# Kernel tuning notes

Hardware: AMD Instinct MI355X
Metric: run time of the kernel (lower is better)

Reference implementation:

```python
import jax, jax.numpy as jnp
import numpy as np

N_NODES = 50000
IN_CH = 512
OUT_CH = 128
N_EDGES = 1_600_000


def setup_inputs() -> dict:
    key = jax.random.key(0)
    k1, k2, k3, k4 = jax.random.split(key, 4)
    x = jax.random.normal(k1, (N_NODES, IN_CH), dtype=jnp.float32)
    edge_index = jax.random.randint(k2, (2, N_EDGES), 0, N_NODES, dtype=jnp.int64)
    # GCNConv params (weight [in, out], bias [out]); decoder Linear(out, in, bias=False) -> weight [in, out] used as z @ W_dec
    W_enc = jax.random.normal(k3, (IN_CH, OUT_CH), dtype=jnp.float32) * 0.05
    b_enc = jnp.zeros((OUT_CH,), dtype=jnp.float32)
    W_dec = jax.random.normal(k4, (OUT_CH, IN_CH), dtype=jnp.float32) * 0.05
    return {"x": x, "edge_index": edge_index, "W_enc": W_enc, "b_enc": b_enc, "W_dec": W_dec}


def reference(x, edge_index, W_enc, b_enc, W_dec):
    N = x.shape[0]
    # --- GCNConv: add self-loops, symmetric normalization, gather-scale-scatter ---
    loops = jnp.arange(N, dtype=edge_index.dtype)
    src = jnp.concatenate([edge_index[0], loops])  # message sources
    dst = jnp.concatenate([edge_index[1], loops])  # aggregation targets
    deg = jax.ops.segment_sum(jnp.ones_like(dst, dtype=x.dtype), dst, num_segments=N)
    deg_inv_sqrt = jnp.where(deg > 0, jax.lax.rsqrt(jnp.maximum(deg, 1.0)), 0.0)
    norm = deg_inv_sqrt[src] * deg_inv_sqrt[dst]  # [E+N]
    xw = x @ W_enc                                 # [N, OUT]
    msg = xw[src] * norm[:, None]                  # gather + scale
    z = jax.ops.segment_sum(msg, dst, num_segments=N) + b_enc  # scatter-add
    # --- decode head: relu -> linear (no bias) -> softmax over features ---
    z = jax.nn.relu(z)
    logits = z @ W_dec                             # [N, IN]
    return jax.nn.softmax(logits, axis=1)
```

## Files before the change

kernel.cpp:

```cpp
#include <hip/hip_runtime.h>
#include <stdint.h>

#define NN   50000
#define INC  512
#define OUTC 128
#define NB   782
#define CAP  4096
#define NWG  256

typedef unsigned int  uint;
typedef unsigned short u16;
typedef short bf16x8 __attribute__((ext_vector_type(8)));
typedef float f32x4  __attribute__((ext_vector_type(4)));
typedef u16   u16x8  __attribute__((ext_vector_type(8)));
typedef u16   u16x4  __attribute__((ext_vector_type(4)));

__device__ __forceinline__ u16 f2bf(float f) {
  uint u = __float_as_uint(f);
  u += 0x7fffu + ((u >> 16) & 1u);
  return (u16)(u >> 16);
}
__device__ __forceinline__ float bflo(uint v) { return __uint_as_float(v << 16); }
__device__ __forceinline__ float bfhi(uint v) { return __uint_as_float(v & 0xffff0000u); }

__device__ __forceinline__ void gl_lds16(const void* g, void* l) {
  __builtin_amdgcn_global_load_lds(
      (const __attribute__((address_space(1))) uint*)g,
      (__attribute__((address_space(3))) uint*)l, 16, 0, 0);
}

__global__ __launch_bounds__(256) void k_scatter_pairs(const int* __restrict__ src,
                                                       const int* __restrict__ dst, int E,
                                                       uint* __restrict__ bucket_cursor,
                                                       uint* __restrict__ pairs) {
  __shared__ uint hist[NB];
  __shared__ uint base[NB];
  __shared__ uint cur[NB];
  const int t = threadIdx.x;
  const int chunk = (E + NWG - 1) / NWG;
  const int e0 = blockIdx.x * chunk;
  const int e1 = min(e0 + chunk, E);

  for (int i = t; i < NB; i += 256) hist[i] = 0;
  __syncthreads();
  for (int e = e0 + t; e < e1; e += 256) {
    int b = dst[e] >> 6;
    atomicAdd(&hist[b], 1u);
  }
  __syncthreads();
  for (int i = t; i < NB; i += 256) {
    uint c = hist[i];
    base[i] = c ? atomicAdd(&bucket_cursor[i * 16], c) : 0u;
    cur[i] = 0;
  }
  __syncthreads();
  for (int e = e0 + t; e < e1; e += 256) {
    int d = dst[e];
    int b = d >> 6;
    uint r = atomicAdd(&cur[b], 1u);
    uint off = base[b] + r;
    if (off < CAP) pairs[(size_t)b * CAP + off] = (uint)src[e] | ((uint)(d & 63) << 16);
  }
}

__global__ __launch_bounds__(256) void k_sort(const uint* __restrict__ bucket_cursor,
                                              const uint* __restrict__ pairs,
                                              uint* __restrict__ csr,
                                              uint* __restrict__ rs_packed,
                                              float* __restrict__ dis) {
  __shared__ uint plist[CAP];
  __shared__ uint slist[CAP];
  __shared__ uint cnt[64], pfx[64], cur[64];
  const int b = blockIdx.x, t = threadIdx.x;
  uint n_e = bucket_cursor[b * 16]; if (n_e > CAP) n_e = CAP;

  if (t < 64) cnt[t] = 0;
  __syncthreads();
  for (uint e = t; e < n_e; e += 256) {
    uint v = pairs[(size_t)b * CAP + e];
    plist[e] = v;
    atomicAdd(&cnt[(v >> 16) & 63u], 1u);
  }
  __syncthreads();
  if (t == 0) {
    uint run = 0;
    for (int i = 0; i < 64; ++i) { pfx[i] = run; run += cnt[i]; }
  }
  __syncthreads();
  if (t < 64) {
    cur[t] = pfx[t];
    int n = b * 64 + t;
    if (n < NN) {
      rs_packed[n] = pfx[t] | (cnt[t] << 16);
      dis[n] = rsqrtf((float)cnt[t] + 1.0f);
    }
  }
  __syncthreads();
  for (uint e = t; e < n_e; e += 256) {
    uint v = plist[e];
    uint pos = atomicAdd(&cur[(v >> 16) & 63u], 1u);
    slist[pos] = v & 0xffffu;
  }
  __syncthreads();
  for (uint e = t; e < n_e; e += 256) csr[(size_t)b * CAP + e] = slist[e];
}

__global__ __launch_bounds__(256) void k_prep(const float* __restrict__ We,
                                              const float* __restrict__ Wd,
                                              uint8_t* __restrict__ oE,
                                              uint8_t* __restrict__ oD) {
  __shared__ float t[4096];
  const int tid = threadIdx.x;
  if (blockIdx.x < 16) {
    const int k0 = blockIdx.x * 32;
#pragma unroll
    for (int r = 0; r < 16; ++r) {
      int e = r * 256 + tid;
      int kk = e >> 7, n = e & 127;
      t[kk * 128 + n] = We[(size_t)(k0 + kk) * 128 + n];
    }
    __syncthreads();
#pragma unroll
    for (int it = 0; it < 2; ++it) {
      int item = it * 256 + tid;
      int n = item & 127, kc = item >> 7;
      int kg = k0 + kc * 8;
      int q = kg >> 7, kin = kg & 127;
      u16x8 p;
#pragma unroll
      for (int j = 0; j < 8; ++j) p[j] = f2bf(t[(kc * 8 + j) * 128 + n]);
      *(u16x8*)(oE + q * 32768 + ((((uint)n * 256) + (uint)kin * 2) ^ (uint)((n & 7) << 4))) = p;
    }
  } else {
    const int n0 = (blockIdx.x - 16) * 32;
#pragma unroll
    for (int r = 0; r < 16; ++r) {
      int e = r * 256 + tid;
      int k = e >> 5, nl = e & 31;
      t[k * 32 + nl] = Wd[(size_t)k * 512 + n0 + nl];
    }
    __syncthreads();
#pragma unroll
    for (int it = 0; it < 2; ++it) {
      int item = it * 256 + tid;
      int nl = item & 31, kc = item >> 5;
      int n = n0 + nl;
      int c = n >> 7, nin = n & 127;
      u16x8 p;
#pragma unroll
      for (int j = 0; j < 8; ++j) p[j] = f2bf(t[(kc * 8 + j) * 32 + nl]);
      *(u16x8*)(oD + c * 32768 + ((((uint)nin * 256) + (uint)kc * 16) ^ (uint)((nin & 7) << 4))) = p;
    }
  }
}

__global__ __launch_bounds__(256, 2) void k_gemm1(const float* __restrict__ x,
                                                  const uint8_t* __restrict__ WtE,
                                                  const float* __restrict__ dis,
                                                  u16* __restrict__ xws) {
  __shared__ __align__(16) uint8_t lds[49152];
  uint8_t* WL = lds;
  uint8_t* XL = lds + 32768;
  const int tid = threadIdx.x, lane = tid & 63, wv = tid >> 6;
  const int lane15 = lane & 15, laneh = lane >> 4;
  const int rb = blockIdx.x * 128;

  f32x4 acc[2][8];
#pragma unroll
  for (int m = 0; m < 2; ++m)
#pragma unroll
    for (int n = 0; n < 8; ++n) acc[m][n] = (f32x4){0.f, 0.f, 0.f, 0.f};

  const int srow = tid >> 1;
  int grow = rb + srow; if (grow >= NN) grow = NN - 1;
  const int khalf = (tid & 1) * 32;
  const uint xb  = (uint)srow * 128 + (uint)khalf * 2;
  const uint xsw = (uint)((srow & 7) << 4);
  const int ar0 = wv * 32 + lane15, ar1 = ar0 + 16;

  for (int q = 0; q < 4; ++q) {
    __syncthreads();
    { const uint8_t* s = WtE + q * 32768;
#pragma unroll
      for (int i = 0; i < 8; ++i)
        gl_lds16(s + tid * 16 + i * 4096, WL + tid * 16 + i * 4096); }
#pragma unroll
    for (int step = 0; step < 2; ++step) {
      if (step) __syncthreads();
      const float4* xs = (const float4*)(x + (size_t)grow * INC + q * 128 + step * 64 + khalf);
      float4 v[8];
#pragma unroll
      for (int j = 0; j < 8; ++j) v[j] = xs[j];
#pragma unroll
      for (int j = 0; j < 8; ++j) {
        u16x4 p; p.x = f2bf(v[j].x); p.y = f2bf(v[j].y); p.z = f2bf(v[j].z); p.w = f2bf(v[j].w);
        *(u16x4*)(XL + ((xb + j * 8) ^ xsw)) = p;
      }
      __syncthreads();
#pragma unroll
      for (int kk = 0; kk < 2; ++kk) {
        bf16x8 a0 = *(const bf16x8*)(XL + (((uint)ar0 * 128 + kk * 64 + laneh * 16) ^ (uint)((ar0 & 7) << 4)));
        bf16x8 a1 = *(const bf16x8*)(XL + (((uint)ar1 * 128 + kk * 64 + laneh * 16) ^ (uint)((ar1 & 7) << 4)));
#pragma unroll
        for (int nf = 0; nf < 8; ++nf) {
          int n = nf * 16 + lane15;
          bf16x8 b = *(const bf16x8*)(WL + (((uint)n * 256 + step * 128 + kk * 64 + laneh * 16) ^ (uint)((n & 7) << 4)));
          acc[0][nf] = __builtin_amdgcn_mfma_f32_16x16x32_bf16(a0, b, acc[0][nf], 0, 0, 0);
          acc[1][nf] = __builtin_amdgcn_mfma_f32_16x16x32_bf16(a1, b, acc[1][nf], 0, 0, 0);
        }
      }
    }
  }
#pragma unroll
  for (int m = 0; m < 2; ++m) {
#pragma unroll
    for (int r = 0; r < 4; ++r) {
      int row = rb + wv * 32 + m * 16 + laneh * 4 + r;
      if (row < NN) {
        float dv = dis[row];
#pragma unroll
        for (int nf = 0; nf < 8; ++nf)
          xws[(size_t)row * 128 + nf * 16 + lane15] = f2bf(acc[m][nf][r] * dv);
      }
    }
  }
}

__global__ __launch_bounds__(128) void k_aggregate(const u16* __restrict__ xws,
                                                   const float* __restrict__ dis,
                                                   const uint* __restrict__ rs_packed,
                                                   const uint* __restrict__ csr,
                                                   const float* __restrict__ bias,
                                                   uint8_t* __restrict__ zsw) {
  const int i = blockIdx.x * 2 + (threadIdx.x >> 6);
  const int lane = threadIdx.x & 63;
  const uint v = rs_packed[i];
  const uint s0 = (uint)(i >> 6) * CAP + (v & 0xffffu);
  const uint s1 = s0 + (v >> 16);

  float a0 = 0.f, a1 = 0.f;
  uint j = s0;
  for (; j + 7 < s1; j += 8) {
    uint idx[8], vv[8];
#pragma unroll
    for (int t = 0; t < 8; ++t) idx[t] = csr[j + t];
#pragma unroll
    for (int t = 0; t < 8; ++t) vv[t] = *(const uint*)(xws + (size_t)idx[t] * 128 + lane * 2);
#pragma unroll
    for (int t = 0; t < 8; ++t) { a0 += bflo(vv[t]); a1 += bfhi(vv[t]); }
  }
  for (; j < s1; ++j) {
    uint vv = *(const uint*)(xws + (size_t)csr[j] * 128 + lane * 2);
    a0 += bflo(vv); a1 += bfhi(vv);
  }
  uint vs = *(const uint*)(xws + (size_t)i * 128 + lane * 2);
  float di = dis[i];
  float2 bb = *(const float2*)(bias + lane * 2);
  float z0 = fmaxf(di * (a0 + bflo(vs)) + bb.x, 0.f);
  float z1 = fmaxf(di * (a1 + bfhi(vs)) + bb.y, 0.f);
  uint pk = (uint)f2bf(z0) | ((uint)f2bf(z1) << 16);
  *(uint*)(zsw + ((((uint)i * 256) + (uint)lane * 4) ^ (uint)((i & 7) << 4))) = pk;
}

__global__ __launch_bounds__(256, 2) void k_decode(const uint8_t* __restrict__ zsw,
                                                   const uint8_t* __restrict__ WtD,
                                                   float* __restrict__ out) {
  __shared__ __align__(16) uint8_t lds[49152];
  uint8_t* ZL = lds;
  uint8_t* WL = lds + 16384;
  const int tid = threadIdx.x, lane = tid & 63, wv = tid >> 6;
  const int lane15 = lane & 15, laneh = lane >> 4;
  const int rb = blockIdx.x * 64;

  { const uint8_t* s = zsw + (size_t)rb * 256;
#pragma unroll
    for (int i = 0; i < 4; ++i)
      gl_lds16(s + tid * 16 + i * 4096, ZL + tid * 16 + i * 4096); }

  f32x4 acc[32];
#pragma unroll
  for (int f = 0; f < 32; ++f) acc[f] = (f32x4){0.f, 0.f, 0.f, 0.f};

  const int zr = wv * 16 + lane15;
  bf16x8 a[4];

#pragma unroll
  for (int c = 0; c < 4; ++c) {
    if (c) __syncthreads();
    { const uint8_t* s = WtD + c * 32768;
#pragma unroll
      for (int i = 0; i < 8; ++i)
        gl_lds16(s + tid * 16 + i * 4096, WL + tid * 16 + i * 4096); }
    __syncthreads();
    if (c == 0) {
#pragma unroll
      for (int s = 0; s < 4; ++s)
        a[s] = *(const bf16x8*)(ZL + (((uint)zr * 256 + s * 64 + laneh * 16) ^ (uint)((zr & 7) << 4)));
    }
#pragma unroll
    for (int nf = 0; nf < 8; ++nf) {
      int n = nf * 16 + lane15;
      uint nb = (uint)n * 256 + laneh * 16, nsw = (uint)((n & 7) << 4);
#pragma unroll
      for (int s = 0; s < 4; ++s) {
        bf16x8 bfr = *(const bf16x8*)(WL + ((nb + s * 64) ^ nsw));
        acc[c * 8 + nf] = __builtin_amdgcn_mfma_f32_16x16x32_bf16(a[s], bfr, acc[c * 8 + nf], 0, 0, 0);
      }
    }
  }

#pragma unroll
  for (int r = 0; r < 4; ++r) {
    float m = acc[0][r];
#pragma unroll
    for (int f = 1; f < 32; ++f) m = fmaxf(m, acc[f][r]);
    m = fmaxf(m, __shfl_xor(m, 1)); m = fmaxf(m, __shfl_xor(m, 2));
    m = fmaxf(m, __shfl_xor(m, 4)); m = fmaxf(m, __shfl_xor(m, 8));
    float sum = 0.f;
#pragma unroll
    for (int f = 0; f < 32; ++f) { acc[f][r] = __expf(acc[f][r] - m); sum += acc[f][r]; }
    sum += __shfl_xor(sum, 1); sum += __shfl_xor(sum, 2);
    sum += __shfl_xor(sum, 4); sum += __shfl_xor(sum, 8);
    float inv = 1.0f / sum;
    int row = rb + wv * 16 + laneh * 4 + r;
    if (row < NN) {
      float* op = out + (size_t)row * INC + lane15;
#pragma unroll
      for (int f = 0; f < 32; ++f)
        op[(f >> 3) * 128 + (f & 7) * 16] = acc[f][r] * inv;
    }
  }
}

extern "C" void kernel_launch(void* const* d_in, const int* in_sizes, int n_in,
                              void* d_out, int out_size, void* d_ws, size_t ws_size,
                              hipStream_t stream) {
  const float* x     = (const float*)d_in[0];
  const int*   ei    = (const int*)d_in[1];
  const float* W_enc = (const float*)d_in[2];
  const float* b_enc = (const float*)d_in[3];
  const float* W_dec = (const float*)d_in[4];
  float* out = (float*)d_out;

  const int E = in_sizes[1] / 2;
  const int* esrc = ei;
  const int* edst = ei + E;

  uint8_t* ws = (uint8_t*)d_ws;
  uint*  bucket_cursor = (uint*)(ws);
  uint*  pairs         = (uint*)(ws + 0x10000);
  uint*  csr           = (uint*)(ws + 0xC80000);
  uint*  rs_packed     = (uint*)(ws + 0x1900000);
  float* dis           = (float*)(ws + 0x1940000);
  uint8_t* WtE         = ws + 0x1980000;
  uint8_t* WtD         = ws + 0x19A0000;
  u16*   xws           = (u16*)(ws + 0x19C0000);
  uint8_t* zsw         = ws + 0x2600000;

  hipMemsetAsync(bucket_cursor, 0, NB * 64, stream);
  k_scatter_pairs<<<NWG, 256, 0, stream>>>(esrc, edst, E, bucket_cursor, pairs);
  k_sort         <<<NB, 256, 0, stream>>>(bucket_cursor, pairs, csr, rs_packed, dis);
  k_prep         <<<32, 256, 0, stream>>>(W_enc, W_dec, WtE, WtD);
  k_gemm1        <<<(NN + 127) / 128, 256, 0, stream>>>(x, WtE, dis, xws);
  k_aggregate    <<<NN / 2, 128, 0, stream>>>(xws, dis, rs_packed, csr, b_enc, zsw);
  k_decode       <<<(NN + 63) / 64, 256, 0, stream>>>(zsw, WtD, out);
}
```

Baseline: 339.7 us.

## Make encoder and decoder GEMMs persistent with whole weight resident in LDS

Both GEMM kernels become persistent: 256 blocks of 512 threads each load the full 128 KB bf16 weight into LDS once. Each wave then walks a contiguous range of 16-row fragments, loading activations straight from global into registers with no LDS staging and no per-K barriers. The encoder also uses the packed v_cvt_pk_bf16_f32 conversion. This removes repeated weight reloads and barrier overhead, at the cost of one block per CU because of the LDS footprint, less latency hiding for the global activation loads, and uncoalesced per-lane row reads of x.

```diff
diff --git a/kernel.cpp b/kernel.cpp
--- a/kernel.cpp
+++ b/kernel.cpp
@@ -7,13 +7,13 @@
 #define NB   782
 #define CAP  4096
 #define NWG  256
+#define NFRAG 3125
 
 typedef unsigned int  uint;
 typedef unsigned short u16;
 typedef short bf16x8 __attribute__((ext_vector_type(8)));
 typedef float f32x4  __attribute__((ext_vector_type(4)));
 typedef u16   u16x8  __attribute__((ext_vector_type(8)));
-typedef u16   u16x4  __attribute__((ext_vector_type(4)));
 
 __device__ __forceinline__ u16 f2bf(float f) {
   uint u = __float_as_uint(f);
@@ -22,6 +22,18 @@
 }
 __device__ __forceinline__ float bflo(uint v) { return __uint_as_float(v << 16); }
 __device__ __forceinline__ float bfhi(uint v) { return __uint_as_float(v & 0xffff0000u); }
+
+__device__ __forceinline__ uint pkbf(float lo, float hi) {
+  uint r;
+  asm("v_cvt_pk_bf16_f32 %0, %1, %2" : "=v"(r) : "v"(lo), "v"(hi));
+  return r;
+}
+__device__ __forceinline__ bf16x8 pack8(float4 a, float4 b) {
+  union { uint u[4]; bf16x8 v; } c;
+  c.u[0] = pkbf(a.x, a.y); c.u[1] = pkbf(a.z, a.w);
+  c.u[2] = pkbf(b.x, b.y); c.u[3] = pkbf(b.z, b.w);
+  return c.v;
+}
 
 __device__ __forceinline__ void gl_lds16(const void* g, void* l) {
   __builtin_amdgcn_global_load_lds(
@@ -154,74 +166,60 @@
   }
 }
 
-__global__ __launch_bounds__(256, 2) void k_gemm1(const float* __restrict__ x,
+__global__ __launch_bounds__(512, 2) void k_gemm1(const float* __restrict__ x,
                                                   const uint8_t* __restrict__ WtE,
                                                   const float* __restrict__ dis,
                                                   u16* __restrict__ xws) {
-  __shared__ __align__(16) uint8_t lds[49152];
-  uint8_t* WL = lds;
-  uint8_t* XL = lds + 32768;
+  __shared__ __align__(16) uint8_t WL[131072];
   const int tid = threadIdx.x, lane = tid & 63, wv = tid >> 6;
   const int lane15 = lane & 15, laneh = lane >> 4;
-  const int rb = blockIdx.x * 128;
-
-  f32x4 acc[2][8];
-#pragma unroll
-  for (int m = 0; m < 2; ++m)
-#pragma unroll
-    for (int n = 0; n < 8; ++n) acc[m][n] = (f32x4){0.f, 0.f, 0.f, 0.f};
-
-  const int srow = tid >> 1;
-  int grow = rb + srow; if (grow >= NN) grow = NN - 1;
-  const int khalf = (tid & 1) * 32;
-  const uint xb  = (uint)srow * 128 + (uint)khalf * 2;
-  const uint xsw = (uint)((srow & 7) << 4);
-  const int ar0 = wv * 32 + lane15, ar1 = ar0 + 16;
-
-  for (int q = 0; q < 4; ++q) {
-    __syncthreads();
-    { const uint8_t* s = WtE + q * 32768;
-#pragma unroll
-      for (int i = 0; i < 8; ++i)
-        gl_lds16(s + tid * 16 + i * 4096, WL + tid * 16 + i * 4096); }
-#pragma unroll
-    for (int step = 0; step < 2; ++step) {
-      if (step) __syncthreads();
-      const float4* xs = (const float4*)(x + (size_t)grow * INC + q * 128 + step * 64 + khalf);
-      float4 v[8];
-#pragma unroll
-      for (int j = 0; j < 8; ++j) v[j] = xs[j];
-#pragma unroll
-      for (int j = 0; j < 8; ++j) {
-        u16x4 p; p.x = f2bf(v[j].x); p.y = f2bf(v[j].y); p.z = f2bf(v[j].z); p.w = f2bf(v[j].w);
-        *(u16x4*)(XL + ((xb + j * 8) ^ xsw)) = p;
+
+#pragma unroll
+  for (int i = 0; i < 16; ++i)
+    gl_lds16(WtE + tid * 16 + i * 8192, WL + tid * 16 + i * 8192);
+  __syncthreads();
+
+  const int s = blockIdx.x * 8 + wv;
+  const int f0 = (s * NFRAG) >> 11, f1 = ((s + 1) * NFRAG) >> 11;
+
+  for (int f = f0; f < f1; ++f) {
+    const float* xr = x + (size_t)(f * 16 + lane15) * INC + laneh * 8;
+    bf16x8 a[16];
+#pragma unroll
+    for (int g = 0; g < 2; ++g) {
+      float4 u[16];
+#pragma unroll
+      for (int sl = 0; sl < 8; ++sl) {
+        u[sl * 2]     = *(const float4*)(xr + (g * 8 + sl) * 32);
+        u[sl * 2 + 1] = *(const float4*)(xr + (g * 8 + sl) * 32 + 4);
       }
-      __syncthreads();
-#pragma unroll
-      for (int kk = 0; kk < 2; ++kk) {
-        bf16x8 a0 = *(const bf16x8*)(XL + (((uint)ar0 * 128 + kk * 64 + laneh * 16) ^ (uint)((ar0 & 7) << 4)));
-        bf16x8 a1 = *(const bf16x8*)(XL + (((uint)ar1 * 128 + kk * 64 + laneh * 16) ^ (uint)((ar1 & 7) << 4)));
-#pragma unroll
-        for (int nf = 0; nf < 8; ++nf) {
-          int n = nf * 16 + lane15;
-          bf16x8 b = *(const bf16x8*)(WL + (((uint)n * 256 + step * 128 + kk * 64 + laneh * 16) ^ (uint)((n & 7) << 4)));
-          acc[0][nf] = __builtin_amdgcn_mfma_f32_16x16x32_bf16(a0, b, acc[0][nf], 0, 0, 0);
-          acc[1][nf] = __builtin_amdgcn_mfma_f32_16x16x32_bf16(a1, b, acc[1][nf], 0, 0, 0);
-        }
+#pragma unroll
+      for (int sl = 0; sl < 8; ++sl)
+        a[g * 8 + sl] = pack8(u[sl * 2], u[sl * 2 + 1]);
+    }
+
+    f32x4 acc[8];
+#pragma unroll
+    for (int nf = 0; nf < 8; ++nf) acc[nf] = (f32x4){0.f, 0.f, 0.f, 0.f};
+
+#pragma unroll
+    for (int sl = 0; sl < 16; ++sl) {
+      const uint kb = ((uint)(sl >> 2) << 15) + (uint)(sl & 3) * 64 + (uint)laneh * 16;
+#pragma unroll
+      for (int nf = 0; nf < 8; ++nf) {
+        int n = nf * 16 + lane15;
+        bf16x8 b = *(const bf16x8*)(WL + ((kb + (uint)n * 256) ^ (uint)((n & 7) << 4)));
+        acc[nf] = __builtin_amdgcn_mfma_f32_16x16x32_bf16(a[sl], b, acc[nf], 0, 0, 0);
       }
     }
-  }
-#pragma unroll
-  for (int m = 0; m < 2; ++m) {
+
 #pragma unroll
     for (int r = 0; r < 4; ++r) {
-      int row = rb + wv * 32 + m * 16 + laneh * 4 + r;
-      if (row < NN) {
-        float dv = dis[row];
-#pragma unroll
-        for (int nf = 0; nf < 8; ++nf)
-          xws[(size_t)row * 128 + nf * 16 + lane15] = f2bf(acc[m][nf][r] * dv);
-      }
+      int row = f * 16 + laneh * 4 + r;
+      float dv = dis[row];
+#pragma unroll
+      for (int nf = 0; nf < 8; ++nf)
+        xws[(size_t)row * 128 + nf * 16 + lane15] = f2bf(acc[nf][r] * dv);
     }
   }
 }
@@ -262,72 +260,63 @@
   *(uint*)(zsw + ((((uint)i * 256) + (uint)lane * 4) ^ (uint)((i & 7) << 4))) = pk;
 }
 
-__global__ __launch_bounds__(256, 2) void k_decode(const uint8_t* __restrict__ zsw,
+__global__ __launch_bounds__(512, 2) void k_decode(const uint8_t* __restrict__ zsw,
                                                    const uint8_t* __restrict__ WtD,
                                                    float* __restrict__ out) {
-  __shared__ __align__(16) uint8_t lds[49152];
-  uint8_t* ZL = lds;
-  uint8_t* WL = lds + 16384;
+  __shared__ __align__(16) uint8_t WL[131072];
   const int tid = threadIdx.x, lane = tid & 63, wv = tid >> 6;
   const int lane15 = lane & 15, laneh = lane >> 4;
-  const int rb = blockIdx.x * 64;
-
-  { const uint8_t* s = zsw + (size_t)rb * 256;
-#pragma unroll
-    for (int i = 0; i < 4; ++i)
-      gl_lds16(s + tid * 16 + i * 4096, ZL + tid * 16 + i * 4096); }
-
-  f32x4 acc[32];
-#pragma unroll
-  for (int f = 0; f < 32; ++f) acc[f] = (f32x4){0.f, 0.f, 0.f, 0.f};
-
-  const int zr = wv * 16 + lane15;
-  bf16x8 a[4];
-
-#pragma unroll
-  for (int c = 0; c < 4; ++c) {
-    if (c) __syncthreads();
-    { const uint8_t* s = WtD + c * 32768;
-#pragma unroll
-      for (int i = 0; i < 8; ++i)
-        gl_lds16(s + tid * 16 + i * 4096, WL + tid * 16 + i * 4096); }
-    __syncthreads();
-    if (c == 0) {
-#pragma unroll
-      for (int s = 0; s < 4; ++s)
-        a[s] = *(const bf16x8*)(ZL + (((uint)zr * 256 + s * 64 + laneh * 16) ^ (uint)((zr & 7) << 4)));
-    }
-#pragma unroll
-    for (int nf = 0; nf < 8; ++nf) {
+
+#pragma unroll
+  for (int i = 0; i < 16; ++i)
+    gl_lds16(WtD + tid * 16 + i * 8192, WL + tid * 16 + i * 8192);
+  __syncthreads();
+
+  const int s = blockIdx.x * 8 + wv;
+  const int f0 = (s * NFRAG) >> 11, f1 = ((s + 1) * NFRAG) >> 11;
+
+  for (int f = f0; f < f1; ++f) {
+    const int zr = f * 16 + lane15;
+    const uint zsz = (uint)((zr & 7) << 4);
+    bf16x8 a[4];
+#pragma unroll
+    for (int s2 = 0; s2 < 4; ++s2)
+      a[s2] = *(const bf16x8*)(zsw + (((uint)zr * 256 + s2 * 64 + laneh * 16) ^ zsz));
+
+    f32x4 acc[32];
+#pragma unroll
+    for (int nf = 0; nf < 32; ++nf) acc[nf] = (f32x4){0.f, 0.f, 0.f, 0.f};
+
+#pragma unroll
+    for (int nf = 0; nf < 32; ++nf) {
       int n = nf * 16 + lane15;
-      uint nb = (uint)n * 256 + laneh * 16, nsw = (uint)((n & 7) << 4);
-#pragma unroll
-      for (int s = 0; s < 4; ++s) {
-        bf16x8 bfr = *(const bf16x8*)(WL + ((nb + s * 64) ^ nsw));
-        acc[c * 8 + nf] = __builtin_amdgcn_mfma_f32_16x16x32_bf16(a[s], bfr, acc[c * 8 + nf], 0, 0, 0);
+      uint nb = ((uint)(n >> 7) << 15) + (uint)(n & 127) * 256 + (uint)laneh * 16;
+      uint nsw = (uint)((n & 7) << 4);
+#pragma unroll
+      for (int s2 = 0; s2 < 4; ++s2) {
+        bf16x8 b = *(const bf16x8*)(WL + ((nb + s2 * 64) ^ nsw));
+        acc[nf] = __builtin_amdgcn_mfma_f32_16x16x32_bf16(a[s2], b, acc[nf], 0, 0, 0);
       }
     }
-  }
-
-#pragma unroll
-  for (int r = 0; r < 4; ++r) {
-    float m = acc[0][r];
-#pragma unroll
-    for (int f = 1; f < 32; ++f) m = fmaxf(m, acc[f][r]);
-    m = fmaxf(m, __shfl_xor(m, 1)); m = fmaxf(m, __shfl_xor(m, 2));
-    m = fmaxf(m, __shfl_xor(m, 4)); m = fmaxf(m, __shfl_xor(m, 8));
-    float sum = 0.f;
-#pragma unroll
-    for (int f = 0; f < 32; ++f) { acc[f][r] = __expf(acc[f][r] - m); sum += acc[f][r]; }
-    sum += __shfl_xor(sum, 1); sum += __shfl_xor(sum, 2);
-    sum += __shfl_xor(sum, 4); sum += __shfl_xor(sum, 8);
-    float inv = 1.0f / sum;
-    int row = rb + wv * 16 + laneh * 4 + r;
-    if (row < NN) {
+
+#pragma unroll
+    for (int r = 0; r < 4; ++r) {
+      float m = acc[0][r];
+#pragma unroll
+      for (int nf = 1; nf < 32; ++nf) m = fmaxf(m, acc[nf][r]);
+      m = fmaxf(m, __shfl_xor(m, 1)); m = fmaxf(m, __shfl_xor(m, 2));
+      m = fmaxf(m, __shfl_xor(m, 4)); m = fmaxf(m, __shfl_xor(m, 8));
+      float sum = 0.f;
+#pragma unroll
+      for (int nf = 0; nf < 32; ++nf) { acc[nf][r] = __expf(acc[nf][r] - m); sum += acc[nf][r]; }
+      sum += __shfl_xor(sum, 1); sum += __shfl_xor(sum, 2);
+      sum += __shfl_xor(sum, 4); sum += __shfl_xor(sum, 8);
+      float inv = 1.0f / sum;
+      int row = f * 16 + laneh * 4 + r;
       float* op = out + (size_t)row * INC + lane15;
 #pragma unroll
-      for (int f = 0; f < 32; ++f)
-        op[(f >> 3) * 128 + (f & 7) * 16] = acc[f][r] * inv;
+      for (int nf = 0; nf < 32; ++nf)
+        op[nf * 16] = acc[nf][r] * inv;
     }
   }
 }
@@ -361,7 +350,7 @@
   k_scatter_pairs<<<NWG, 256, 0, stream>>>(esrc, edst, E, bucket_cursor, pairs);
   k_sort         <<<NB, 256, 0, stream>>>(bucket_cursor, pairs, csr, rs_packed, dis);
   k_prep         <<<32, 256, 0, stream>>>(W_enc, W_dec, WtE, WtD);
-  k_gemm1        <<<(NN + 127) / 128, 256, 0, stream>>>(x, WtE, dis, xws);
+  k_gemm1        <<<256, 512, 0, stream>>>(x, WtE, dis, xws);
   k_aggregate    <<<NN / 2, 128, 0, stream>>>(xws, dis, rs_packed, csr, b_enc, zsw);
-  k_decode       <<<(NN + 63) / 64, 256, 0, stream>>>(zsw, WtD, out);
-}
+  k_decode       <<<256, 512, 0, stream>>>(zsw, WtD, out);
+}
```

Result: slower. 366.1 us (+7.8%).
